# Performance work log

Hardware: AMD Instinct MI355X
Metric: run time of the kernel (lower is better)

## Reference

```python
import jax, jax.numpy as jnp
import numpy as np
from jax import lax


def _conv(x, w, b):
    # NCHW valid conv, stride 1 (torch Conv2d semantics)
    y = lax.conv_general_dilated(x, w, (1, 1), 'VALID',
                                 dimension_numbers=('NCHW', 'OIHW', 'NCHW'))
    return y + b[None, :, None, None]


def _maxpool(x, k, s):
    return lax.reduce_window(x, -jnp.inf, lax.max, (1, 1, k, k), (1, 1, s, s), 'VALID')


def _lin(x, w, b):
    # torch nn.Linear: y = x @ W^T + b, applied to last dim
    return x @ w.T + b


def setup_inputs() -> dict:
    key = jax.random.key(0)
    ks = jax.random.split(key, 21)
    def f(i, shape, scale):
        return jax.random.normal(ks[i], shape, dtype=jnp.float32) * scale
    return {
        'x': f(0, (512, 1, 28, 28), 1.0),
        'c1_w': f(1, (50, 1, 3, 3), 0.33), 'c1_b': f(2, (50,), 0.1),
        'c2_w': f(3, (50, 50, 3, 3), 0.047), 'c2_b': f(4, (50,), 0.05),
        'c3_w': f(5, (50, 50, 3, 3), 0.047), 'c3_b': f(6, (50,), 0.05),
        'l1_w': f(7, (500, 50), 0.14), 'l1_b': f(8, (500,), 0.05),
        'l2_w': f(9, (10, 500), 0.045), 'l2_b': f(10, (10,), 0.05),
        'd1_w': f(11, (3, 8450), 0.011), 'd1_b': f(12, (3,), 0.05),
        'd2_w': f(13, (2, 1250), 0.028), 'd2_b': f(14, (2,), 0.05),
        'c1c3_w': f(15, (13, 13), 0.28), 'c1c3_b': f(16, (13,), 0.05),
        'c1l1_w': f(17, (500, 1), 1.0), 'c1l1_b': f(18, (500,), 0.05),
        'c2l1_w': f(19, (500, 5), 0.45), 'c2l1_b': f(20, (500,), 0.05),
    }


def reference(x, c1_w, c1_b, c2_w, c2_b, c3_w, c3_b, l1_w, l1_b, l2_w, l2_b,
              d1_w, d1_b, d2_w, d2_b, c1c3_w, c1c3_b, c1l1_w, c1l1_b,
              c2l1_w, c2l1_b):
    B = x.shape[0]
    # stage 1: conv1 + relu + pool2 -> [B,50,13,13]
    h1 = _maxpool(jax.nn.relu(_conv(x, c1_w, c1_b)), 2, 2)
    # router 1 (argmax over 3 branches): 0 -> conv2 path, 1 -> c1_c3 path, 2 -> early-exit linear path
    d1 = jnp.argmax(_lin(h1.reshape(B, -1), d1_w, d1_b), axis=1)  # [B]
    # branch l11 (d1==2): pool7 -> [B,50,1,1], Linear(1->500) on last dim -> [B,50,1,500]
    l11 = _lin(_maxpool(h1, 7, 7), c1l1_w, c1l1_b)
    # branch c3-direct (d1==1): Linear(13->13) on last dim, then conv3+relu+pool2 -> [B,50,5,5]
    c33 = _lin(h1, c1c3_w, c1c3_b)
    c3d = _maxpool(jax.nn.relu(_conv(c33, c3_w, c3_b)), 2, 2)
    # branch c2 (d1==0): conv2+relu+pool2 -> [B,50,5,5]
    h2 = _maxpool(jax.nn.relu(_conv(h1, c2_w, c2_b)), 2, 2)
    # router 2 (argmax over 2 sub-branches)
    d2 = jnp.argmax(_lin(h2.reshape(B, -1), d2_w, d2_b), axis=1)  # [B]
    # sub-branch c32 (d2==0): conv3+relu+pool2 -> [B,50,1,1]
    c32 = _maxpool(jax.nn.relu(_conv(h2, c3_w, c3_b)), 2, 2)
    # sub-branch l12 (d2==1): Linear(5->500) on last dim -> [B,50,5,500], pool3 -> [B,50,1,166]
    l12 = _maxpool(_lin(h2, c2l1_w, c2l1_b), 3, 3)

    def head(t):
        # original: .view(-1, 50) -> linear1/relu/linear2/log_softmax; row-major flatten per sample
        r = t.reshape(B, -1, 50)
        return jax.nn.log_softmax(_lin(jax.nn.relu(_lin(r, l1_w, l1_b)), l2_w, l2_b), axis=-1)

    dt = x.dtype
    m_l11 = (d1 == 2).astype(dt)[:, None, None]
    m_c3d = (d1 == 1).astype(dt)[:, None, None]
    m_c32 = ((d1 == 0) & (d2 == 0)).astype(dt)[:, None, None]
    m_l12 = ((d1 == 0) & (d2 == 1)).astype(dt)[:, None, None]
    # dense masked combine (static-shape equivalent of the gather/compute/concat dispatch);
    # branch order matches the original concatenation: l11, l12, c32, c3-direct
    out = jnp.concatenate([head(l11) * m_l11, head(l12) * m_l12,
                           head(c32) * m_c32, head(c3d) * m_c3d], axis=1)  # [B,692,10]
    return out, d1, d2
```

## Files before the change

kernel.cpp:

```cpp
#include <hip/hip_runtime.h>
#include <hip/hip_bf16.h>
#include <math.h>

#define BB 512
#define CC 50

typedef __attribute__((ext_vector_type(8))) __bf16 bf16x8;
typedef __attribute__((ext_vector_type(4))) float f32x4;

__global__ void k_zero(float* __restrict__ out, int n4) {
  int i = blockIdx.x * 256 + threadIdx.x;
  if (i < n4) {
    float4 z = {0.f, 0.f, 0.f, 0.f};
    ((float4*)out)[i] = z;
  }
}

__global__ void k_pack(const float* __restrict__ l1w, const float* __restrict__ l1b,
                       const float* __restrict__ l2w,
                       __bf16* __restrict__ W1p, float* __restrict__ W2t) {
  int idx = blockIdx.x * 256 + threadIdx.x;
  if (idx < 512 * 64) {
    int j = idx >> 6, k = idx & 63;
    float v = 0.f;
    if (j < 500) {
      if (k < 50) v = l1w[j * 50 + k];
      else if (k == 50) v = l1b[j];
    }
    W1p[idx] = (__bf16)v;
  } else if (idx < 512 * 64 + 512 * 12) {
    int i2 = idx - 512 * 64;
    int j = i2 / 12, n = i2 % 12;
    W2t[i2] = (n < 10 && j < 500) ? l2w[n * 500 + j] : 0.f;
  }
}

__global__ void k_conv1(const float* __restrict__ x, const float* __restrict__ w,
                        const float* __restrict__ bias, float* __restrict__ h1) {
  int idx = blockIdx.x * 256 + threadIdx.x;
  if (idx >= BB * CC * 169) return;
  int b = idx / (CC * 169);
  int rem = idx % (CC * 169);
  int c = rem / 169;
  int p = rem % 169;
  int py = p / 13, px = p % 13;
  const float* xi = x + b * 784;
  float wr[9];
#pragma unroll
  for (int i = 0; i < 9; i++) wr[i] = w[c * 9 + i];
  float m = -INFINITY;
#pragma unroll
  for (int dy = 0; dy < 2; dy++)
#pragma unroll
    for (int dx = 0; dx < 2; dx++) {
      int y0 = 2 * py + dy, x0 = 2 * px + dx;
      float s = 0.f;
#pragma unroll
      for (int ky = 0; ky < 3; ky++)
#pragma unroll
        for (int kx = 0; kx < 3; kx++)
          s += xi[(y0 + ky) * 28 + x0 + kx] * wr[ky * 3 + kx];
      m = fmaxf(m, s);
    }
  h1[idx] = fmaxf(m + bias[c], 0.f);
}

__global__ void k_d1p7(const float* __restrict__ h1, const float* __restrict__ w,
                       const float* __restrict__ bias, int* __restrict__ d1i,
                       float* __restrict__ outd1, float* __restrict__ p7) {
  int b = blockIdx.x, t = threadIdx.x;
  const float* hb = h1 + b * 8450;
  float s0 = 0.f, s1 = 0.f, s2 = 0.f;
  for (int i = t; i < 8450; i += 256) {
    float v = hb[i];
    s0 += v * w[i];
    s1 += v * w[8450 + i];
    s2 += v * w[16900 + i];
  }
#pragma unroll
  for (int off = 32; off >= 1; off >>= 1) {
    s0 += __shfl_down(s0, off);
    s1 += __shfl_down(s1, off);
    s2 += __shfl_down(s2, off);
  }
  __shared__ float red[4][3];
  if ((t & 63) == 0) { red[t >> 6][0] = s0; red[t >> 6][1] = s1; red[t >> 6][2] = s2; }
  __syncthreads();
  if (t == 0) {
    float l0 = bias[0], l1v = bias[1], l2v = bias[2];
    for (int wv = 0; wv < 4; wv++) { l0 += red[wv][0]; l1v += red[wv][1]; l2v += red[wv][2]; }
    int idx = 0; float best = l0;
    if (l1v > best) { best = l1v; idx = 1; }
    if (l2v > best) { best = l2v; idx = 2; }
    d1i[b] = idx;
    outd1[b] = (float)idx;
  }
  if (t < 50) {
    const float* hp = hb + t * 169;
    float m = -INFINITY;
#pragma unroll
    for (int y = 0; y < 7; y++)
#pragma unroll
      for (int x = 0; x < 7; x++) m = fmaxf(m, hp[y * 13 + x]);
    p7[b * 50 + t] = m;
  }
}

template <int MODE>
__global__ __launch_bounds__(256) void k_conv5(const float* __restrict__ in,
                                               const float* __restrict__ w,
                                               const float* __restrict__ bias,
                                               const int* __restrict__ d1i,
                                               const float* __restrict__ w13,
                                               const float* __restrict__ b13,
                                               float* __restrict__ out) {
  int b = blockIdx.x;
  if (MODE == 1 && d1i[b] != 1) return;
  __shared__ float sh[50 * 260];
  __shared__ float w13s[182];
  int t = threadIdx.x;
  for (int i = t; i < 8450; i += 256) {
    int ic = i / 169, r = i % 169;
    int row = r / 13, xx = r % 13;
    sh[ic * 260 + row * 20 + xx] = in[b * 8450 + i];
  }
  if (MODE == 1) {
    for (int i = t; i < 182; i += 256) w13s[i] = (i < 169) ? w13[i] : b13[i - 169];
  }
  __syncthreads();
  if (MODE == 1) {
    for (int p = t; p < 650; p += 256) {
      float* row = sh + (p / 13) * 260 + (p % 13) * 20;
      float r[13];
#pragma unroll
      for (int k = 0; k < 13; k++) r[k] = row[k];
#pragma unroll
      for (int xx = 0; xx < 13; xx++) {
        float s = w13s[169 + xx];
#pragma unroll
        for (int k = 0; k < 13; k++) s += r[k] * w13s[xx * 13 + k];
        row[xx] = s;
      }
    }
    __syncthreads();
  }
  if (t >= 250) return;
  int oc = t / 5, py = t % 5;
  float acc[5][4];
#pragma unroll
  for (int i = 0; i < 5; i++)
#pragma unroll
    for (int j = 0; j < 4; j++) acc[i][j] = 0.f;
  const float* wb = w + oc * 450;
  for (int ic = 0; ic < 50; ic++) {
    float wv[9];
#pragma unroll
    for (int i = 0; i < 9; i++) wv[i] = wb[ic * 9 + i];
    float r[4][13];
    const float* rp = sh + ic * 260 + 2 * py * 20;
#pragma unroll
    for (int rr = 0; rr < 4; rr++) {
      const float* p4 = rp + rr * 20;
      float4 q0 = *(const float4*)(p4);
      float4 q1 = *(const float4*)(p4 + 4);
      float4 q2 = *(const float4*)(p4 + 8);
      r[rr][0] = q0.x; r[rr][1] = q0.y; r[rr][2] = q0.z; r[rr][3] = q0.w;
      r[rr][4] = q1.x; r[rr][5] = q1.y; r[rr][6] = q1.z; r[rr][7] = q1.w;
      r[rr][8] = q2.x; r[rr][9] = q2.y; r[rr][10] = q2.z; r[rr][11] = q2.w;
      r[rr][12] = p4[12];
    }
#pragma unroll
    for (int px = 0; px < 5; px++)
#pragma unroll
      for (int dy = 0; dy < 2; dy++)
#pragma unroll
        for (int dx = 0; dx < 2; dx++) {
          float s = acc[px][dy * 2 + dx];
          int x0 = 2 * px + dx;
#pragma unroll
          for (int ky = 0; ky < 3; ky++)
#pragma unroll
            for (int kx = 0; kx < 3; kx++)
              s += r[dy + ky][x0 + kx] * wv[ky * 3 + kx];
          acc[px][dy * 2 + dx] = s;
        }
  }
  float bs = bias[oc];
#pragma unroll
  for (int px = 0; px < 5; px++) {
    float m = fmaxf(fmaxf(acc[px][0], acc[px][1]), fmaxf(acc[px][2], acc[px][3]));
    out[((b * 50 + oc) * 5 + py) * 5 + px] = fmaxf(m + bs, 0.f);
  }
}

__global__ __launch_bounds__(256) void k_d2c(const float* __restrict__ h2,
                                             const float* __restrict__ d2w,
                                             const float* __restrict__ d2b,
                                             const float* __restrict__ c3w,
                                             const float* __restrict__ c3b,
                                             const float* __restrict__ c2l1w,
                                             const float* __restrict__ c2l1b,
                                             const int* __restrict__ d1i,
                                             int* __restrict__ d2i,
                                             float* __restrict__ outd2,
                                             float* __restrict__ c32,
                                             float* __restrict__ l12) {
  int b = blockIdx.x, t = threadIdx.x;
  __shared__ float hs[1250];
  __shared__ float wls[2500];
  __shared__ float bls[500];
  __shared__ float red[4][2];
  __shared__ int sd2;
  for (int i = t; i < 1250; i += 256) hs[i] = h2[b * 1250 + i];
  __syncthreads();
  float s0 = 0.f, s1 = 0.f;
  for (int i = t; i < 1250; i += 256) {
    float v = hs[i];
    s0 += v * d2w[i];
    s1 += v * d2w[1250 + i];
  }
#pragma unroll
  for (int off = 32; off >= 1; off >>= 1) {
    s0 += __shfl_down(s0, off);
    s1 += __shfl_down(s1, off);
  }
  if ((t & 63) == 0) { red[t >> 6][0] = s0; red[t >> 6][1] = s1; }
  __syncthreads();
  if (t == 0) {
    float l0 = d2b[0] + red[0][0] + red[1][0] + red[2][0] + red[3][0];
    float l1v = d2b[1] + red[0][1] + red[1][1] + red[2][1] + red[3][1];
    int idx = (l1v > l0) ? 1 : 0;
    d2i[b] = idx;
    outd2[b] = (float)idx;
    sd2 = idx;
  }
  __syncthreads();
  int d2v = sd2;
  if (d1i[b] != 0) return;
  if (d2v == 0) {
    if (t < 50) {
      const float* wb = c3w + t * 450;
      float a[4] = {0.f, 0.f, 0.f, 0.f};
      for (int ic = 0; ic < 50; ic++) {
        float r[4][4];
#pragma unroll
        for (int y = 0; y < 4; y++)
#pragma unroll
          for (int xx = 0; xx < 4; xx++) r[y][xx] = hs[ic * 25 + y * 5 + xx];
        float wv[9];
#pragma unroll
        for (int i = 0; i < 9; i++) wv[i] = wb[ic * 9 + i];
#pragma unroll
        for (int py = 0; py < 2; py++)
#pragma unroll
          for (int px = 0; px < 2; px++) {
            float s = a[py * 2 + px];
#pragma unroll
            for (int ky = 0; ky < 3; ky++)
#pragma unroll
              for (int kx = 0; kx < 3; kx++)
                s += r[py + ky][px + kx] * wv[ky * 3 + kx];
            a[py * 2 + px] = s;
          }
      }
      float m = fmaxf(fmaxf(a[0], a[1]), fmaxf(a[2], a[3]));
      c32[b * 50 + t] = fmaxf(m + c3b[t], 0.f);
    }
  } else {
    for (int i = t; i < 2500; i += 256) wls[i] = c2l1w[i];
    for (int i = t; i < 500; i += 256) bls[i] = c2l1b[i];
    __syncthreads();
    for (int o = t; o < 8300; o += 256) {
      int c = o / 166, tt = o % 166;
      const float* hb = hs + c * 25;
      float m = -INFINITY;
#pragma unroll
      for (int i = 0; i < 3; i++) {
        float a0 = hb[i * 5 + 0], a1 = hb[i * 5 + 1], a2 = hb[i * 5 + 2],
              a3 = hb[i * 5 + 3], a4 = hb[i * 5 + 4];
#pragma unroll
        for (int dj = 0; dj < 3; dj++) {
          int j = 3 * tt + dj;
          const float* wj = wls + j * 5;
          float s = bls[j] + a0 * wj[0] + a1 * wj[1] + a2 * wj[2] + a3 * wj[3] + a4 * wj[4];
          m = fmaxf(m, s);
        }
      }
      l12[b * 8300 + o] = m;
    }
  }
}

__global__ void k_count(const int* __restrict__ d1i, const int* __restrict__ d2i,
                        int* __restrict__ off, int* __restrict__ ntot) {
  __shared__ int s[512];
  int t = threadIdx.x;
  int d1 = d1i[t], d2 = d2i[t];
  int nr = (d1 == 2) ? 500 : (d1 == 1) ? 25 : (d2 == 1) ? 166 : 1;
  s[t] = nr;
  __syncthreads();
  for (int o = 1; o < 512; o <<= 1) {
    int v = (t >= o) ? s[t - o] : 0;
    __syncthreads();
    s[t] += v;
    __syncthreads();
  }
  off[t] = s[t] - nr;
  if (t == 511) ntot[0] = s[511];
}

__global__ void k_fill(const int* __restrict__ d1i, const int* __restrict__ d2i,
                       const int* __restrict__ off, int* __restrict__ rowtab) {
  int b = blockIdx.x;
  int d1 = d1i[b], d2 = d2i[b];
  int nr, rstart;
  if (d1 == 2)      { nr = 500; rstart = 0; }
  else if (d1 == 1) { nr = 25;  rstart = 667; }
  else if (d2 == 1) { nr = 166; rstart = 500; }
  else              { nr = 1;   rstart = 666; }
  int o = off[b];
  for (int i = threadIdx.x; i < nr; i += 256)
    rowtab[o + i] = (b << 10) | (rstart + i);
}

__global__ __launch_bounds__(256) void k_headc(
    const float* __restrict__ c3d, const float* __restrict__ c32,
    const float* __restrict__ p7, const float* __restrict__ l12buf,
    const int* __restrict__ rowtab, const int* __restrict__ ntotp,
    const __bf16* __restrict__ W1p, const float* __restrict__ W2t,
    const float* __restrict__ l2b,
    const float* __restrict__ c1l1w, const float* __restrict__ c1l1b,
    float* __restrict__ out) {
  int ntot = ntotp[0];
  int t = threadIdx.x;
  int wv = t >> 6, lane = t & 63;
  int lr = lane & 15, lg = lane >> 4;
  int rowbase = blockIdx.x * 256 + wv * 64;
  if (rowbase >= ntot) return;

  bf16x8 a1[4][2];
#pragma unroll
  for (int mt = 0; mt < 4; ++mt) {
    int row = rowbase + mt * 16 + lr;
    int rowc = (row < ntot) ? row : (ntot - 1);
    int e = rowtab[rowc];
    int b = e >> 10, orow = e & 1023;
    float pv = 0.f;
    const float* wsrc = nullptr;
    const float* bsrc = nullptr;
    const float* src = nullptr;
    bool isl11 = (orow < 500);
    if (isl11) {
      pv = p7[b * 50 + orow / 10];
      int q = (orow % 10) * 50;
      wsrc = c1l1w + q;
      bsrc = c1l1b + q;
    } else if (orow < 666) {
      src = l12buf + b * 8300 + (orow - 500) * 50;
    } else if (orow == 666) {
      src = c32 + b * 50;
    } else {
      src = c3d + b * 1250 + (orow - 667) * 50;
    }
#pragma unroll
    for (int ks = 0; ks < 2; ++ks) {
      float v[8];
      int k0 = ks * 32 + lg * 8;
      if (ks == 0 || lg < 2) {
        if (isl11) {
#pragma unroll
          for (int i = 0; i < 8; i += 2) {
            float2 wq = *(const float2*)(wsrc + k0 + i);
            float2 bq = *(const float2*)(bsrc + k0 + i);
            v[i] = pv * wq.x + bq.x;
            v[i + 1] = pv * wq.y + bq.y;
          }
        } else {
#pragma unroll
          for (int i = 0; i < 8; i += 2) {
            float2 q = *(const float2*)(src + k0 + i);
            v[i] = q.x; v[i + 1] = q.y;
          }
        }
      } else if (lg == 2) {
        float2 q;
        if (isl11) {
          float2 wq = *(const float2*)(wsrc + 48);
          float2 bq = *(const float2*)(bsrc + 48);
          q.x = pv * wq.x + bq.x; q.y = pv * wq.y + bq.y;
        } else {
          q = *(const float2*)(src + 48);
        }
        v[0] = q.x; v[1] = q.y; v[2] = 1.0f;
        v[3] = 0.f; v[4] = 0.f; v[5] = 0.f; v[6] = 0.f; v[7] = 0.f;
      } else {
#pragma unroll
        for (int i = 0; i < 8; ++i) v[i] = 0.f;
      }
      bf16x8 a;
#pragma unroll
      for (int i = 0; i < 8; ++i) a[i] = (__bf16)v[i];
      a1[mt][ks] = a;
    }
  }

  const __bf16* w1b = W1p + lr * 64 + lg * 8;
  const float* w2base = W2t + lr * 12;
  float acc[4][4][10];
#pragma unroll
  for (int mt = 0; mt < 4; ++mt)
#pragma unroll
    for (int r = 0; r < 4; ++r)
#pragma unroll
      for (int n = 0; n < 10; ++n) acc[mt][r][n] = 0.f;

  bf16x8 c0a = *(const bf16x8*)(w1b);
  bf16x8 c0b = *(const bf16x8*)(w1b + 32);
  bf16x8 c1a = *(const bf16x8*)(w1b + 1024);
  bf16x8 c1b = *(const bf16x8*)(w1b + 1024 + 32);
  float4 n20 = *(const float4*)(w2base);
  float4 n21 = *(const float4*)(w2base + 4);
  float2 n22 = *(const float2*)(w2base + 8);

  for (int jt = 0; jt < 32; ++jt) {
    bf16x8 b0 = c0a, b1 = c0b;
    c0a = c1a; c0b = c1b;
    if (jt + 2 < 32) {
      c1a = *(const bf16x8*)(w1b + (jt + 2) * 1024);
      c1b = *(const bf16x8*)(w1b + (jt + 2) * 1024 + 32);
    }
    float w2v[10] = {n20.x, n20.y, n20.z, n20.w, n21.x, n21.y, n21.z, n21.w, n22.x, n22.y};
    if (jt + 1 < 32) {
      const float* wr = w2base + (jt + 1) * 16 * 12;
      n20 = *(const float4*)(wr);
      n21 = *(const float4*)(wr + 4);
      n22 = *(const float2*)(wr + 8);
    }
#pragma unroll
    for (int mt = 0; mt < 4; ++mt) {
      f32x4 dz = {0.f, 0.f, 0.f, 0.f};
      f32x4 h = __builtin_amdgcn_mfma_f32_16x16x32_bf16(a1[mt][0], b0, dz, 0, 0, 0);
      h = __builtin_amdgcn_mfma_f32_16x16x32_bf16(a1[mt][1], b1, h, 0, 0, 0);
#pragma unroll
      for (int r = 0; r < 4; ++r) {
        float hv = fmaxf(h[r], 0.f);
#pragma unroll
        for (int n = 0; n < 10; ++n) acc[mt][r][n] += hv * w2v[n];
      }
    }
  }

#pragma unroll
  for (int mt = 0; mt < 4; ++mt)
#pragma unroll
    for (int r = 0; r < 4; ++r)
#pragma unroll
      for (int n = 0; n < 10; ++n) {
        float v = acc[mt][r][n];
        v += __shfl_xor(v, 1);
        v += __shfl_xor(v, 2);
        v += __shfl_xor(v, 4);
        v += __shfl_xor(v, 8);
        acc[mt][r][n] = v;
      }
  if (lr == 0) {
#pragma unroll
    for (int mt = 0; mt < 4; ++mt) {
#pragma unroll
      for (int r = 0; r < 4; ++r) {
        int row = rowbase + mt * 16 + lg * 4 + r;
        if (row < ntot) {
          int e = rowtab[row];
          int b = e >> 10, orow = e & 1023;
          float o[10];
          float m = -INFINITY;
#pragma unroll
          for (int n = 0; n < 10; ++n) {
            o[n] = acc[mt][r][n] + l2b[n];
            m = fmaxf(m, o[n]);
          }
          float s = 0.f;
#pragma unroll
          for (int n = 0; n < 10; ++n) s += expf(o[n] - m);
          float lse = m + logf(s);
          float* orowp = out + (b * 692 + orow) * 10;
#pragma unroll
          for (int n = 0; n < 10; ++n) orowp[n] = o[n] - lse;
        }
      }
    }
  }
}

extern "C" void kernel_launch(void* const* d_in, const int* in_sizes, int n_in,
                              void* d_out, int out_size, void* d_ws, size_t ws_size,
                              hipStream_t stream) {
  const float* x     = (const float*)d_in[0];
  const float* c1w   = (const float*)d_in[1];
  const float* c1b   = (const float*)d_in[2];
  const float* c2w   = (const float*)d_in[3];
  const float* c2b   = (const float*)d_in[4];
  const float* c3w   = (const float*)d_in[5];
  const float* c3b   = (const float*)d_in[6];
  const float* l1w   = (const float*)d_in[7];
  const float* l1b   = (const float*)d_in[8];
  const float* l2w   = (const float*)d_in[9];
  const float* l2b   = (const float*)d_in[10];
  const float* d1w   = (const float*)d_in[11];
  const float* d1b   = (const float*)d_in[12];
  const float* d2w   = (const float*)d_in[13];
  const float* d2b   = (const float*)d_in[14];
  const float* c13w  = (const float*)d_in[15];
  const float* c13b  = (const float*)d_in[16];
  const float* c1l1w = (const float*)d_in[17];
  const float* c1l1b = (const float*)d_in[18];
  const float* c2l1w = (const float*)d_in[19];
  const float* c2l1b = (const float*)d_in[20];
  float* out = (float*)d_out;

  float* ws  = (float*)d_ws;
  float* h1  = ws;
  float* h2  = h1 + 4326400;
  float* c3d = h2 + 640000;
  float* c32 = c3d + 640000;
  float* p7  = c32 + 25600;
  int*   d1i = (int*)(p7 + 25600);
  int*   d2i = d1i + 512;
  __bf16* W1p = (__bf16*)(d2i + 512);
  float* W2t = (float*)(W1p + 512 * 64);
  int* off    = (int*)(W2t + 512 * 12);
  int* ntot   = off + 512;
  int* rowtab = ntot + 4;
  float* l12buf = h1;

  float* outd1 = out + 512 * 692 * 10;
  float* outd2 = outd1 + 512;

  k_zero<<<3460, 256, 0, stream>>>(out, 885510);
  k_pack<<<153, 256, 0, stream>>>(l1w, l1b, l2w, W1p, W2t);
  k_conv1<<<16900, 256, 0, stream>>>(x, c1w, c1b, h1);
  k_d1p7<<<512, 256, 0, stream>>>(h1, d1w, d1b, d1i, outd1, p7);
  k_conv5<0><<<512, 256, 0, stream>>>(h1, c2w, c2b, d1i, c13w, c13b, h2);
  k_conv5<1><<<512, 256, 0, stream>>>(h1, c3w, c3b, d1i, c13w, c13b, c3d);
  k_d2c<<<512, 256, 0, stream>>>(h2, d2w, d2b, c3w, c3b, c2l1w, c2l1b,
                                 d1i, d2i, outd2, c32, l12buf);
  k_count<<<1, 512, 0, stream>>>(d1i, d2i, off, ntot);
  k_fill<<<512, 256, 0, stream>>>(d1i, d2i, off, rowtab);
  k_headc<<<1024, 256, 0, stream>>>(c3d, c32, p7, l12buf, rowtab, ntot,
                                    W1p, W2t, l2b, c1l1w, c1l1b, out);
}
```

Before: 247.7 us.

## Stage W1 in swizzled LDS and shrink head tiles to 16 rows per wave

The head kernel now stages the packed bf16 first-layer weights into a 32KB XOR-swizzled shared-memory buffer, loaded in two halves, so the four waves of a block share one copy instead of each wave streaming it from global memory. Each wave now handles 16 rows instead of 64, which cuts the accumulator from 160 to 40 floats. Launch bounds ask for 4 blocks per SM and the grid grows to 4000 blocks to cover the rows. The cost is two block-wide barriers and more blocks, each reloading the full weight set into LDS for only 64 rows.

After: 481.0 us. +94.2%, slower.

```diff
diff --git a/kernel.cpp b/kernel.cpp
--- a/kernel.cpp
+++ b/kernel.cpp
@@ -323,7 +323,11 @@
     rowtab[o + i] = (b << 10) | (rstart + i);
 }
 
-__global__ __launch_bounds__(256) void k_headc(
+__device__ __forceinline__ int swz(int byteoff) {
+  return byteoff ^ (((byteoff >> 7) & 7) << 4);
+}
+
+__global__ __launch_bounds__(256, 4) void k_headc(
     const float* __restrict__ c3d, const float* __restrict__ c32,
     const float* __restrict__ p7, const float* __restrict__ l12buf,
     const int* __restrict__ rowtab, const int* __restrict__ ntotp,
@@ -332,35 +336,36 @@
     const float* __restrict__ c1l1w, const float* __restrict__ c1l1b,
     float* __restrict__ out) {
   int ntot = ntotp[0];
+  int blkbase = blockIdx.x * 64;
+  if (blkbase >= ntot) return;
+
+  __shared__ __align__(16) char wlds[32768];
   int t = threadIdx.x;
   int wv = t >> 6, lane = t & 63;
   int lr = lane & 15, lg = lane >> 4;
-  int rowbase = blockIdx.x * 256 + wv * 64;
-  if (rowbase >= ntot) return;
-
-  bf16x8 a1[4][2];
-#pragma unroll
-  for (int mt = 0; mt < 4; ++mt) {
-    int row = rowbase + mt * 16 + lr;
-    int rowc = (row < ntot) ? row : (ntot - 1);
-    int e = rowtab[rowc];
-    int b = e >> 10, orow = e & 1023;
+
+  int row = blkbase + wv * 16 + lr;
+  int rowc = (row < ntot) ? row : (ntot - 1);
+  int e = rowtab[rowc];
+  int gb = e >> 10, orow = e & 1023;
+  bf16x8 a1[2];
+  {
     float pv = 0.f;
     const float* wsrc = nullptr;
     const float* bsrc = nullptr;
     const float* src = nullptr;
     bool isl11 = (orow < 500);
     if (isl11) {
-      pv = p7[b * 50 + orow / 10];
+      pv = p7[gb * 50 + orow / 10];
       int q = (orow % 10) * 50;
       wsrc = c1l1w + q;
       bsrc = c1l1b + q;
     } else if (orow < 666) {
-      src = l12buf + b * 8300 + (orow - 500) * 50;
+      src = l12buf + gb * 8300 + (orow - 500) * 50;
     } else if (orow == 666) {
-      src = c32 + b * 50;
+      src = c32 + gb * 50;
     } else {
-      src = c3d + b * 1250 + (orow - 667) * 50;
+      src = c3d + gb * 1250 + (orow - 667) * 50;
     }
 #pragma unroll
     for (int ks = 0; ks < 2; ++ks) {
@@ -400,93 +405,89 @@
       bf16x8 a;
 #pragma unroll
       for (int i = 0; i < 8; ++i) a[i] = (__bf16)v[i];
-      a1[mt][ks] = a;
-    }
-  }
-
-  const __bf16* w1b = W1p + lr * 64 + lg * 8;
+      a1[ks] = a;
+    }
+  }
+
+  float acc[4][10];
+#pragma unroll
+  for (int r = 0; r < 4; ++r)
+#pragma unroll
+    for (int n = 0; n < 10; ++n) acc[r][n] = 0.f;
+
   const float* w2base = W2t + lr * 12;
-  float acc[4][4][10];
-#pragma unroll
-  for (int mt = 0; mt < 4; ++mt)
-#pragma unroll
-    for (int r = 0; r < 4; ++r)
-#pragma unroll
-      for (int n = 0; n < 10; ++n) acc[mt][r][n] = 0.f;
-
-  bf16x8 c0a = *(const bf16x8*)(w1b);
-  bf16x8 c0b = *(const bf16x8*)(w1b + 32);
-  bf16x8 c1a = *(const bf16x8*)(w1b + 1024);
-  bf16x8 c1b = *(const bf16x8*)(w1b + 1024 + 32);
   float4 n20 = *(const float4*)(w2base);
   float4 n21 = *(const float4*)(w2base + 4);
   float2 n22 = *(const float2*)(w2base + 8);
 
-  for (int jt = 0; jt < 32; ++jt) {
-    bf16x8 b0 = c0a, b1 = c0b;
-    c0a = c1a; c0b = c1b;
-    if (jt + 2 < 32) {
-      c1a = *(const bf16x8*)(w1b + (jt + 2) * 1024);
-      c1b = *(const bf16x8*)(w1b + (jt + 2) * 1024 + 32);
-    }
-    float w2v[10] = {n20.x, n20.y, n20.z, n20.w, n21.x, n21.y, n21.z, n21.w, n22.x, n22.y};
-    if (jt + 1 < 32) {
-      const float* wr = w2base + (jt + 1) * 16 * 12;
-      n20 = *(const float4*)(wr);
-      n21 = *(const float4*)(wr + 4);
-      n22 = *(const float2*)(wr + 8);
-    }
-#pragma unroll
-    for (int mt = 0; mt < 4; ++mt) {
-      f32x4 dz = {0.f, 0.f, 0.f, 0.f};
-      f32x4 h = __builtin_amdgcn_mfma_f32_16x16x32_bf16(a1[mt][0], b0, dz, 0, 0, 0);
-      h = __builtin_amdgcn_mfma_f32_16x16x32_bf16(a1[mt][1], b1, h, 0, 0, 0);
+  for (int p = 0; p < 2; ++p) {
+    if (p > 0) __syncthreads();
+    {
+      const char* src = (const char*)W1p + p * 32768 + t * 128;
+#pragma unroll
+      for (int i = 0; i < 8; ++i) {
+        float4 q = *(const float4*)(src + i * 16);
+        *(float4*)(wlds + swz(t * 128 + i * 16)) = q;
+      }
+    }
+    __syncthreads();
+#pragma unroll
+    for (int jl = 0; jl < 16; ++jl) {
+      int jt = p * 16 + jl;
+      int boff = jl * 2048 + lr * 128 + lg * 16;
+      bf16x8 b0 = *(const bf16x8*)(wlds + swz(boff));
+      bf16x8 b1 = *(const bf16x8*)(wlds + swz(boff + 64));
+      float w2v[10] = {n20.x, n20.y, n20.z, n20.w, n21.x, n21.y, n21.z, n21.w, n22.x, n22.y};
+      if (jt + 1 < 32) {
+        const float* wr = w2base + (jt + 1) * 16 * 12;
+        n20 = *(const float4*)(wr);
+        n21 = *(const float4*)(wr + 4);
+        n22 = *(const float2*)(wr + 8);
+      }
+      f32x4 h = {0.f, 0.f, 0.f, 0.f};
+      h = __builtin_amdgcn_mfma_f32_16x16x32_bf16(a1[0], b0, h, 0, 0, 0);
+      h = __builtin_amdgcn_mfma_f32_16x16x32_bf16(a1[1], b1, h, 0, 0, 0);
 #pragma unroll
       for (int r = 0; r < 4; ++r) {
         float hv = fmaxf(h[r], 0.f);
 #pragma unroll
-        for (int n = 0; n < 10; ++n) acc[mt][r][n] += hv * w2v[n];
-      }
-    }
-  }
-
-#pragma unroll
-  for (int mt = 0; mt < 4; ++mt)
-#pragma unroll
-    for (int r = 0; r < 4; ++r)
-#pragma unroll
-      for (int n = 0; n < 10; ++n) {
-        float v = acc[mt][r][n];
-        v += __shfl_xor(v, 1);
-        v += __shfl_xor(v, 2);
-        v += __shfl_xor(v, 4);
-        v += __shfl_xor(v, 8);
-        acc[mt][r][n] = v;
-      }
+        for (int n = 0; n < 10; ++n) acc[r][n] += hv * w2v[n];
+      }
+    }
+  }
+
+#pragma unroll
+  for (int r = 0; r < 4; ++r)
+#pragma unroll
+    for (int n = 0; n < 10; ++n) {
+      float v = acc[r][n];
+      v += __shfl_xor(v, 1);
+      v += __shfl_xor(v, 2);
+      v += __shfl_xor(v, 4);
+      v += __shfl_xor(v, 8);
+      acc[r][n] = v;
+    }
   if (lr == 0) {
 #pragma unroll
-    for (int mt = 0; mt < 4; ++mt) {
-#pragma unroll
-      for (int r = 0; r < 4; ++r) {
-        int row = rowbase + mt * 16 + lg * 4 + r;
-        if (row < ntot) {
-          int e = rowtab[row];
-          int b = e >> 10, orow = e & 1023;
-          float o[10];
-          float m = -INFINITY;
-#pragma unroll
-          for (int n = 0; n < 10; ++n) {
-            o[n] = acc[mt][r][n] + l2b[n];
-            m = fmaxf(m, o[n]);
-          }
-          float s = 0.f;
-#pragma unroll
-          for (int n = 0; n < 10; ++n) s += expf(o[n] - m);
-          float lse = m + logf(s);
-          float* orowp = out + (b * 692 + orow) * 10;
-#pragma unroll
-          for (int n = 0; n < 10; ++n) orowp[n] = o[n] - lse;
+    for (int r = 0; r < 4; ++r) {
+      int rw = blkbase + wv * 16 + lg * 4 + r;
+      if (rw < ntot) {
+        int e2 = rowtab[rw];
+        int b2 = e2 >> 10, orow2 = e2 & 1023;
+        float o[10];
+        float m = -INFINITY;
+#pragma unroll
+        for (int n = 0; n < 10; ++n) {
+          o[n] = acc[r][n] + l2b[n];
+          m = fmaxf(m, o[n]);
         }
+        float s = 0.f;
+#pragma unroll
+        for (int n = 0; n < 10; ++n) s += expf(o[n] - m);
+        float lse = m + logf(s);
+        float* orowp = out + (b2 * 692 + orow2) * 10;
+#pragma unroll
+        for (int n = 0; n < 10; ++n) orowp[n] = o[n] - lse;
       }
     }
   }
@@ -546,6 +547,6 @@
                                  d1i, d2i, outd2, c32, l12buf);
   k_count<<<1, 512, 0, stream>>>(d1i, d2i, off, ntot);
   k_fill<<<512, 256, 0, stream>>>(d1i, d2i, off, rowtab);
-  k_headc<<<1024, 256, 0, stream>>>(c3d, c32, p7, l12buf, rowtab, ntot,
+  k_headc<<<4000, 256, 0, stream>>>(c3d, c32, p7, l12buf, rowtab, ntot,
                                     W1p, W2t, l2b, c1l1w, c1l1b, out);
 }
```
